# Performance work log

Measured on AMD Instinct MI355X. Metric: run time of the kernel, lower is better.

The kernel has to match this reference:

```python
import jax, jax.numpy as jnp
import numpy as np

B, T, S, C, H, F = 8, 1024, 256, 1024, 16, 4096
D = C // H  # head_dim = 64
EPS = 1e-5


def layernorm(x, g, b):
    mu = jnp.mean(x, axis=-1, keepdims=True)
    var = jnp.var(x, axis=-1, keepdims=True)
    return (x - mu) * jax.lax.rsqrt(var + EPS) * g + b


def setup_inputs() -> dict:
    key = jax.random.key(0)
    ks = jax.random.split(key, 16)
    s = lambda fan_in: 1.0 / np.sqrt(fan_in)
    return {
        "x": jax.random.normal(ks[0], (B, T, C), jnp.float32),
        "context": jax.random.normal(ks[1], (B, S, C), jnp.float32),
        # LayerNorms
        "ln1_g": jnp.ones((C,)), "ln1_b": jnp.zeros((C,)),
        "ln2_g": jnp.ones((C,)), "ln2_b": jnp.zeros((C,)),
        "ln3_g": jnp.ones((C,)), "ln3_b": jnp.zeros((C,)),
        # causal self-attention (qkv has no bias, proj has bias)
        "W_qkv": jax.random.normal(ks[2], (C, 3 * C), jnp.float32) * s(C),
        "W_sproj": jax.random.normal(ks[3], (C, C), jnp.float32) * s(C),
        "b_sproj": jnp.zeros((C,)),
        # cross-attention
        "W_q": jax.random.normal(ks[4], (C, C), jnp.float32) * s(C),
        "W_kv": jax.random.normal(ks[5], (C, 2 * C), jnp.float32) * s(C),
        "W_cproj": jax.random.normal(ks[6], (C, C), jnp.float32) * s(C),
        "b_cproj": jnp.zeros((C,)),
        # FFN
        "W_ff1": jax.random.normal(ks[7], (C, F), jnp.float32) * s(C),
        "b_ff1": jnp.zeros((F,)),
        "W_ff2": jax.random.normal(ks[8], (F, C), jnp.float32) * s(F),
        "b_ff2": jnp.zeros((C,)),
    }


def _split_heads(t):  # [B, L, C] -> [B, H, L, D]
    return t.reshape(t.shape[0], t.shape[1], H, D).transpose(0, 2, 1, 3)


def _merge_heads(t):  # [B, H, L, D] -> [B, L, C]
    return t.transpose(0, 2, 1, 3).reshape(t.shape[0], t.shape[2], C)


def gpt_block(x, context, ln1_g, ln1_b, ln2_g, ln2_b, ln3_g, ln3_b,
              W_qkv, W_sproj, b_sproj, W_q, W_kv, W_cproj, b_cproj,
              W_ff1, b_ff1, W_ff2, b_ff2):
    scale = 1.0 / np.sqrt(D)

    # --- causal self-attention (pre-norm) ---
    h = layernorm(x, ln1_g, ln1_b)
    qkv = h @ W_qkv                       # [B, T, 3C]
    q, k, v = jnp.split(qkv, 3, axis=-1)
    q, k, v = _split_heads(q), _split_heads(k), _split_heads(v)
    attn = jnp.einsum("bhtd,bhsd->bhts", q, k) * scale   # [B, H, T, T]
    causal = jnp.tril(jnp.ones((T, T), dtype=bool))
    attn = jnp.where(causal, attn, -jnp.inf)
    attn = jax.nn.softmax(attn, axis=-1)
    out = jnp.einsum("bhts,bhsd->bhtd", attn, v)
    x = x + (_merge_heads(out) @ W_sproj + b_sproj)

    # --- cross-attention (pre-norm) ---
    h = layernorm(x, ln2_g, ln2_b)
    q = _split_heads(h @ W_q)             # [B, H, T, D]
    kv = context @ W_kv                   # [B, S, 2C]
    k, v = jnp.split(kv, 2, axis=-1)
    k, v = _split_heads(k), _split_heads(v)
    attn = jax.nn.softmax(jnp.einsum("bhtd,bhsd->bhts", q, k) * scale, axis=-1)
    out = jnp.einsum("bhts,bhsd->bhtd", attn, v)
    x = x + (_merge_heads(out) @ W_cproj + b_cproj)

    # --- FFN (pre-norm, exact GELU) ---
    h = layernorm(x, ln3_g, ln3_b)
    h = jax.nn.gelu(h @ W_ff1 + b_ff1, approximate=False)
    x = x + (h @ W_ff2 + b_ff2)
    return x


def reference(x, context, ln1_g, ln1_b, ln2_g, ln2_b, ln3_g, ln3_b,
              W_qkv, W_sproj, b_sproj, W_q, W_kv, W_cproj, b_cproj,
              W_ff1, b_ff1, W_ff2, b_ff2):
    return gpt_block(x, context, ln1_g, ln1_b, ln2_g, ln2_b, ln3_g, ln3_b,
                     W_qkv, W_sproj, b_sproj, W_q, W_kv, W_cproj, b_cproj,
                     W_ff1, b_ff1, W_ff2, b_ff2)
```

## Files before the change

### kernel.cpp

```cpp
#include <hip/hip_runtime.h>
#include <math.h>

constexpr int B_ = 8, T_ = 1024, S_ = 256, C_ = 1024, H_ = 16, F_ = 4096, D_ = 64;

typedef __attribute__((ext_vector_type(8))) short bf16x8;
typedef __attribute__((ext_vector_type(8))) unsigned short ushort8;
typedef __attribute__((ext_vector_type(4))) unsigned short ushort4v;
typedef __attribute__((ext_vector_type(4))) float f32x4;

__device__ __forceinline__ unsigned short f2bf(float f) {
  union { float f; unsigned u; } c; c.f = f;
  unsigned u = c.u;
  u += 0x7FFFu + ((u >> 16) & 1u);
  return (unsigned short)(u >> 16);
}

__device__ __forceinline__ void gload16(const void* g, void* l) {
  typedef __attribute__((address_space(3))) unsigned int lds_u32;
  typedef __attribute__((address_space(1))) const unsigned int glb_u32;
  __builtin_amdgcn_global_load_lds((glb_u32*)(size_t)g,
                                   (lds_u32*)(unsigned)(size_t)l, 16, 0, 0);
}

__device__ __forceinline__ float gelu_fast(float v) {
  return v / (1.0f + __expf(-1.5957691216057308f * v * (1.0f + 0.044715f * v * v)));
}

__global__ __launch_bounds__(256) void ln_kernel(
    const float* __restrict__ x, const float* __restrict__ g,
    const float* __restrict__ b, unsigned short* __restrict__ out) {
  const int row = blockIdx.x;
  const int t = threadIdx.x;
  const float4 v = reinterpret_cast<const float4*>(x + (size_t)row * C_)[t];
  float sum = v.x + v.y + v.z + v.w;
  float ss  = v.x * v.x + v.y * v.y + v.z * v.z + v.w * v.w;
#pragma unroll
  for (int o = 1; o < 64; o <<= 1) {
    sum += __shfl_xor(sum, o);
    ss  += __shfl_xor(ss, o);
  }
  __shared__ float s1[4], s2[4];
  const int wid = t >> 6;
  if ((t & 63) == 0) { s1[wid] = sum; s2[wid] = ss; }
  __syncthreads();
  sum = s1[0] + s1[1] + s1[2] + s1[3];
  ss  = s2[0] + s2[1] + s2[2] + s2[3];
  const float inv = 1.0f / (float)C_;
  const float mu  = sum * inv;
  const float var = ss * inv - mu * mu;
  const float rstd = rsqrtf(var + 1e-5f);
  const float4 gg = reinterpret_cast<const float4*>(g)[t];
  const float4 bb = reinterpret_cast<const float4*>(b)[t];
  ushort4v o4;
  o4[0] = f2bf((v.x - mu) * rstd * gg.x + bb.x);
  o4[1] = f2bf((v.y - mu) * rstd * gg.y + bb.y);
  o4[2] = f2bf((v.z - mu) * rstd * gg.z + bb.z);
  o4[3] = f2bf((v.w - mu) * rstd * gg.w + bb.w);
  *reinterpret_cast<ushort4v*>(out + (size_t)row * C_ + t * 4) = o4;
}

__global__ __launch_bounds__(256) void wconvT_kernel(
    const float* __restrict__ W, unsigned short* __restrict__ Wt, int K, int N) {
  __shared__ unsigned short Lt[64][72];
  const int tid = threadIdx.x;
  const int n0 = blockIdx.x * 64, k0 = blockIdx.y * 64;
#pragma unroll
  for (int j = 0; j < 4; ++j) {
    const int kk = j * 16 + (tid >> 4);
    const float4 v = *reinterpret_cast<const float4*>(W + (size_t)(k0 + kk) * N + n0 + (tid & 15) * 4);
    const int nn = (tid & 15) * 4;
    Lt[nn + 0][kk] = f2bf(v.x);
    Lt[nn + 1][kk] = f2bf(v.y);
    Lt[nn + 2][kk] = f2bf(v.z);
    Lt[nn + 3][kk] = f2bf(v.w);
  }
  __syncthreads();
  const int rr = tid >> 3, ck = tid & 7;
#pragma unroll
  for (int j = 0; j < 2; ++j) {
    const int n = j * 32 + rr;
    *reinterpret_cast<ushort8*>(Wt + (size_t)(n0 + n) * K + k0 + ck * 8) =
        *reinterpret_cast<const ushort8*>(&Lt[n][ck * 8]);
  }
}

__global__ __launch_bounds__(256) void f2bf_kernel(
    const float* __restrict__ in, unsigned short* __restrict__ o, int n8) {
  const int i = blockIdx.x * 256 + threadIdx.x;
  if (i < n8) {
    const float4 a = *reinterpret_cast<const float4*>(in + (size_t)i * 8);
    const float4 b = *reinterpret_cast<const float4*>(in + (size_t)i * 8 + 4);
    ushort8 r;
    r[0] = f2bf(a.x); r[1] = f2bf(a.y); r[2] = f2bf(a.z); r[3] = f2bf(a.w);
    r[4] = f2bf(b.x); r[5] = f2bf(b.y); r[6] = f2bf(b.z); r[7] = f2bf(b.w);
    *reinterpret_cast<ushort8*>(o + (size_t)i * 8) = r;
  }
}

__global__ __launch_bounds__(256) void vtrans_kernel(
    const unsigned short* __restrict__ src, unsigned short* __restrict__ dst,
    int ldsrc, int Ts) {
  __shared__ unsigned short Lt[64][72];
  const int tid = threadIdx.x;
  const int bh = blockIdx.y, b = bh >> 4, h = bh & 15;
  const int t0 = blockIdx.x * 64;
  const int rr = tid >> 3, ck = tid & 7;
#pragma unroll
  for (int j = 0; j < 2; ++j) {
    const int t = j * 32 + rr;
    const ushort8 v = *reinterpret_cast<const ushort8*>(
        src + (size_t)(b * Ts + t0 + t) * ldsrc + h * 64 + ck * 8);
#pragma unroll
    for (int e = 0; e < 8; ++e) Lt[ck * 8 + e][t] = v[e];
  }
  __syncthreads();
#pragma unroll
  for (int j = 0; j < 2; ++j) {
    const int d = j * 32 + rr;
    *reinterpret_cast<ushort8*>(dst + ((size_t)bh * 64 + d) * Ts + t0 + ck * 8) =
        *reinterpret_cast<const ushort8*>(&Lt[d][ck * 8]);
  }
}

enum { EPI_NONE = 0, EPI_BIAS_RESID = 1, EPI_BIAS_GELU = 2 };

template <int EPI>
__global__ __launch_bounds__(256) void gemm_bf16(
    const unsigned short* __restrict__ A, const unsigned short* __restrict__ Bt,
    const float* __restrict__ bias, const float* __restrict__ resid,
    void* __restrict__ Cout, int M, int N, int K) {
  __shared__ unsigned short As[2][128 * 32];
  __shared__ unsigned short Bs[2][128 * 32];
  const int tid = threadIdx.x;
  const int w = tid >> 6, lane = tid & 63;
  const int ql = lane & 15, g = lane >> 4;
  const int bm = blockIdx.y * 128, bn = blockIdx.x * 128;
  const int wr = w >> 1, wc = w & 1;

  f32x4 acc[4][4] = {};

  const int srow16 = lane >> 2;
  const int skb = lane & 3;

  auto STAGE = [&](int bu, int k0) {
#pragma unroll
    for (int i = 0; i < 2; ++i) {
      const int row = i * 64 + w * 16 + srow16;
      const int kb = skb ^ ((row >> 1) & 3);
      gload16(A + (size_t)(bm + row) * K + k0 + kb * 8,
              (void*)(As[bu] + (i * 64 + w * 16) * 32));
      gload16(Bt + (size_t)(bn + row) * K + k0 + kb * 8,
              (void*)(Bs[bu] + (i * 64 + w * 16) * 32));
    }
  };
  auto COMPUTE = [&](int bu) {
    bf16x8 af[4], bfr[4];
#pragma unroll
    for (int f = 0; f < 4; ++f) {
      const int ra = wr * 64 + f * 16 + ql;
      af[f] = *reinterpret_cast<const bf16x8*>(As[bu] + ra * 32 + (g ^ ((ra >> 1) & 3)) * 8);
      const int rb = wc * 64 + f * 16 + ql;
      bfr[f] = *reinterpret_cast<const bf16x8*>(Bs[bu] + rb * 32 + (g ^ ((rb >> 1) & 3)) * 8);
    }
#pragma unroll
    for (int mf = 0; mf < 4; ++mf)
#pragma unroll
      for (int nf = 0; nf < 4; ++nf)
        acc[mf][nf] = __builtin_amdgcn_mfma_f32_16x16x32_bf16(af[mf], bfr[nf], acc[mf][nf], 0, 0, 0);
  };

  STAGE(0, 0);
  __syncthreads();
  int cur = 0;
  const int NT = K >> 5;
  for (int t = 0; t < NT - 1; ++t) {
    STAGE(cur ^ 1, (t + 1) * 32);
    COMPUTE(cur);
    __syncthreads();
    cur ^= 1;
  }
  COMPUTE(cur);

  float b4[4];
  if (EPI != EPI_NONE) {
#pragma unroll
    for (int nf = 0; nf < 4; ++nf) b4[nf] = bias[bn + wc * 64 + nf * 16 + ql];
  }
#pragma unroll
  for (int mf = 0; mf < 4; ++mf) {
#pragma unroll
    for (int r = 0; r < 4; ++r) {
      const size_t m = (size_t)(bm + wr * 64 + mf * 16 + g * 4 + r);
      const int ncol = bn + wc * 64 + ql;
      if (EPI == EPI_BIAS_RESID) {
        float* op = (float*)Cout + m * N + ncol;
        const float* rp = resid + m * N + ncol;
#pragma unroll
        for (int nf = 0; nf < 4; ++nf)
          op[nf * 16] = acc[mf][nf][r] + b4[nf] + rp[nf * 16];
      } else {
        unsigned short* op = (unsigned short*)Cout + m * N + ncol;
#pragma unroll
        for (int nf = 0; nf < 4; ++nf) {
          float v = acc[mf][nf][r];
          if (EPI == EPI_BIAS_GELU) v = gelu_fast(v + b4[nf]);
          op[nf * 16] = f2bf(v);
        }
      }
    }
  }
}

template <bool CAUSAL>
__global__ __launch_bounds__(256) void attn_mfma(
    const unsigned short* __restrict__ Qb, const unsigned short* __restrict__ Kb,
    const unsigned short* __restrict__ Vt, unsigned short* __restrict__ Ob,
    int Tk, int ldq, int ldk) {
  __shared__ unsigned short Ks[2][64 * 64];
  __shared__ unsigned short Vs[2][64 * 64];
  __shared__ unsigned short Pt[64][72];
  const int tid = threadIdx.x;
  const int w = tid >> 6, lane = tid & 63;
  const int ql = lane & 15, g = lane >> 4;
  const int bh = blockIdx.y, b = bh >> 4, h = bh & 15;
  const int qt = blockIdx.x;
  const int qrow = w * 16 + ql;
  const int qg = qt * 64 + qrow;

  bf16x8 qf0, qf1;
  {
    const unsigned short* qr = Qb + (size_t)(b * T_ + qg) * ldq + h * 64;
    qf0 = *reinterpret_cast<const bf16x8*>(qr + g * 8);
    qf1 = *reinterpret_cast<const bf16x8*>(qr + 32 + g * 8);
  }
  float m_run = -INFINITY, l_run = 0.f;
  f32x4 oacc[4] = {};

  const int nt = CAUSAL ? (qt + 1) : (Tk >> 6);
  const int srow = lane >> 3, skb = lane & 7;

  auto STAGE_KV = [&](int bu, int kt) {
#pragma unroll
    for (int i = 0; i < 2; ++i) {
      const int rloc = i * 32 + w * 8 + srow;
      const int kb = skb ^ (rloc & 7);
      gload16(Kb + (size_t)(b * Tk + kt * 64 + rloc) * ldk + h * 64 + kb * 8,
              (void*)(Ks[bu] + (i * 32 + w * 8) * 64));
      gload16(Vt + ((size_t)bh * 64 + rloc) * Tk + kt * 64 + kb * 8,
              (void*)(Vs[bu] + (i * 32 + w * 8) * 64));
    }
  };

  STAGE_KV(0, 0);
  __syncthreads();
  int cur = 0;

  for (int kt = 0; kt < nt; ++kt) {
    if (kt + 1 < nt) STAGE_KV(cur ^ 1, kt + 1);

    f32x4 sacc[4] = {};
#pragma unroll
    for (int kf = 0; kf < 4; ++kf) {
      const int kr = kf * 16 + ql;
      const int sw = ql & 7;
      const bf16x8 k0v = *reinterpret_cast<const bf16x8*>(Ks[cur] + kr * 64 + ((0 + g) ^ sw) * 8);
      const bf16x8 k1v = *reinterpret_cast<const bf16x8*>(Ks[cur] + kr * 64 + ((4 + g) ^ sw) * 8);
      sacc[kf] = __builtin_amdgcn_mfma_f32_16x16x32_bf16(k0v, qf0, sacc[kf], 0, 0, 0);
      sacc[kf] = __builtin_amdgcn_mfma_f32_16x16x32_bf16(k1v, qf1, sacc[kf], 0, 0, 0);
    }

    float sc[4][4];
    float tmax = -INFINITY;
#pragma unroll
    for (int kf = 0; kf < 4; ++kf)
#pragma unroll
      for (int r = 0; r < 4; ++r) {
        float v = sacc[kf][r] * 0.125f;
        if (CAUSAL) {
          const int key = kt * 64 + kf * 16 + g * 4 + r;
          if (key > qg) v = -INFINITY;
        }
        sc[kf][r] = v;
        tmax = fmaxf(tmax, v);
      }
    tmax = fmaxf(tmax, __shfl_xor(tmax, 16));
    tmax = fmaxf(tmax, __shfl_xor(tmax, 32));
    const float mnew = fmaxf(m_run, tmax);
    const float scl = __expf(m_run - mnew);
    float psum = 0.f;
    unsigned short pb[4][4];
#pragma unroll
    for (int kf = 0; kf < 4; ++kf)
#pragma unroll
      for (int r = 0; r < 4; ++r) {
        const float p = __expf(sc[kf][r] - mnew);
        psum += p;
        pb[kf][r] = f2bf(p);
      }
    psum += __shfl_xor(psum, 16);
    psum += __shfl_xor(psum, 32);
    l_run = l_run * scl + psum;
    m_run = mnew;
#pragma unroll
    for (int df = 0; df < 4; ++df)
#pragma unroll
      for (int r = 0; r < 4; ++r) oacc[df][r] *= scl;
#pragma unroll
    for (int kf = 0; kf < 4; ++kf) {
      ushort4v p4; p4[0] = pb[kf][0]; p4[1] = pb[kf][1]; p4[2] = pb[kf][2]; p4[3] = pb[kf][3];
      *reinterpret_cast<ushort4v*>(&Pt[qrow][kf * 16 + g * 4]) = p4;
    }
    asm volatile("s_waitcnt lgkmcnt(0)" ::: "memory");
    __builtin_amdgcn_s_barrier();

    const bf16x8 p0 = *reinterpret_cast<const bf16x8*>(&Pt[qrow][g * 8]);
    const bf16x8 p1 = *reinterpret_cast<const bf16x8*>(&Pt[qrow][32 + g * 8]);
#pragma unroll
    for (int df = 0; df < 4; ++df) {
      const int vr = df * 16 + ql;
      const int sw = ql & 7;
      const bf16x8 v0 = *reinterpret_cast<const bf16x8*>(Vs[cur] + vr * 64 + ((0 + g) ^ sw) * 8);
      const bf16x8 v1 = *reinterpret_cast<const bf16x8*>(Vs[cur] + vr * 64 + ((4 + g) ^ sw) * 8);
      oacc[df] = __builtin_amdgcn_mfma_f32_16x16x32_bf16(v0, p0, oacc[df], 0, 0, 0);
      oacc[df] = __builtin_amdgcn_mfma_f32_16x16x32_bf16(v1, p1, oacc[df], 0, 0, 0);
    }
    __syncthreads();
    cur ^= 1;
  }

  const float linv = 1.0f / l_run;
  unsigned short* orow = Ob + (size_t)(b * T_ + qg) * C_ + h * 64;
#pragma unroll
  for (int df = 0; df < 4; ++df)
#pragma unroll
    for (int r = 0; r < 4; ++r)
      orow[df * 16 + g * 4 + r] = f2bf(oacc[df][r] * linv);
}

extern "C" void kernel_launch(void* const* d_in, const int* in_sizes, int n_in,
                              void* d_out, int out_size, void* d_ws, size_t ws_size,
                              hipStream_t stream) {
  const float* x    = (const float*)d_in[0];
  const float* ctx  = (const float*)d_in[1];
  const float* ln1g = (const float*)d_in[2];
  const float* ln1b = (const float*)d_in[3];
  const float* ln2g = (const float*)d_in[4];
  const float* ln2b = (const float*)d_in[5];
  const float* ln3g = (const float*)d_in[6];
  const float* ln3b = (const float*)d_in[7];
  const float* Wqkv = (const float*)d_in[8];
  const float* Wsp  = (const float*)d_in[9];
  const float* bsp  = (const float*)d_in[10];
  const float* Wq   = (const float*)d_in[11];
  const float* Wkv  = (const float*)d_in[12];
  const float* Wcp  = (const float*)d_in[13];
  const float* bcp  = (const float*)d_in[14];
  const float* Wf1  = (const float*)d_in[15];
  const float* bf1  = (const float*)d_in[16];
  const float* Wf2  = (const float*)d_in[17];
  const float* bf2  = (const float*)d_in[18];
  float* out = (float*)d_out;

  char* wsb = (char*)d_ws;
  unsigned short* WqkvT = (unsigned short*)(wsb + 0);
  unsigned short* WspT  = (unsigned short*)(wsb + 6291456);
  unsigned short* WqT   = (unsigned short*)(wsb + 8388608);
  unsigned short* WkvT  = (unsigned short*)(wsb + 10485760);
  unsigned short* WcpT  = (unsigned short*)(wsb + 14680064);
  unsigned short* Wf1T  = (unsigned short*)(wsb + 16777216);
  unsigned short* Wf2T  = (unsigned short*)(wsb + 25165824);
  unsigned short* ctxb  = (unsigned short*)(wsb + 33554432);
  unsigned short* lnout = (unsigned short*)(wsb + 37748736);
  unsigned short* attno = (unsigned short*)(wsb + 54525952);
  char* regA = wsb + 71303168;
  unsigned short* qkvb = (unsigned short*)regA;
  unsigned short* VtS  = (unsigned short*)(regA + 50331648);
  unsigned short* qbuf = (unsigned short*)regA;
  unsigned short* kvb  = (unsigned short*)(regA + 16777216);
  unsigned short* VtC  = (unsigned short*)(regA + 25165824);
  unsigned short* ff1o = (unsigned short*)regA;

  const dim3 blk(256);

  wconvT_kernel<<<dim3(48, 16), blk, 0, stream>>>(Wqkv, WqkvT, 1024, 3072);
  wconvT_kernel<<<dim3(16, 16), blk, 0, stream>>>(Wsp, WspT, 1024, 1024);
  wconvT_kernel<<<dim3(16, 16), blk, 0, stream>>>(Wq, WqT, 1024, 1024);
  wconvT_kernel<<<dim3(32, 16), blk, 0, stream>>>(Wkv, WkvT, 1024, 2048);
  wconvT_kernel<<<dim3(16, 16), blk, 0, stream>>>(Wcp, WcpT, 1024, 1024);
  wconvT_kernel<<<dim3(64, 16), blk, 0, stream>>>(Wf1, Wf1T, 1024, 4096);
  wconvT_kernel<<<dim3(16, 64), blk, 0, stream>>>(Wf2, Wf2T, 4096, 1024);
  f2bf_kernel<<<1024, blk, 0, stream>>>(ctx, ctxb, 262144);

  ln_kernel<<<8192, blk, 0, stream>>>(x, ln1g, ln1b, lnout);
  gemm_bf16<EPI_NONE><<<dim3(24, 64), blk, 0, stream>>>(
      lnout, WqkvT, nullptr, nullptr, qkvb, 8192, 3072, 1024);
  vtrans_kernel<<<dim3(16, 128), blk, 0, stream>>>(qkvb + 2048, VtS, 3072, 1024);
  attn_mfma<true><<<dim3(16, 128), blk, 0, stream>>>(
      qkvb, qkvb + 1024, VtS, attno, 1024, 3072, 3072);
  gemm_bf16<EPI_BIAS_RESID><<<dim3(8, 64), blk, 0, stream>>>(
      attno, WspT, bsp, x, out, 8192, 1024, 1024);

  ln_kernel<<<8192, blk, 0, stream>>>(out, ln2g, ln2b, lnout);
  gemm_bf16<EPI_NONE><<<dim3(8, 64), blk, 0, stream>>>(
      lnout, WqT, nullptr, nullptr, qbuf, 8192, 1024, 1024);
  gemm_bf16<EPI_NONE><<<dim3(16, 16), blk, 0, stream>>>(
      ctxb, WkvT, nullptr, nullptr, kvb, 2048, 2048, 1024);
  vtrans_kernel<<<dim3(4, 128), blk, 0, stream>>>(kvb + 1024, VtC, 2048, 256);
  attn_mfma<false><<<dim3(16, 128), blk, 0, stream>>>(
      qbuf, kvb, VtC, attno, 256, 1024, 2048);
  gemm_bf16<EPI_BIAS_RESID><<<dim3(8, 64), blk, 0, stream>>>(
      attno, WcpT, bcp, out, out, 8192, 1024, 1024);

  ln_kernel<<<8192, blk, 0, stream>>>(out, ln3g, ln3b, lnout);
  gemm_bf16<EPI_BIAS_GELU><<<dim3(32, 64), blk, 0, stream>>>(
      lnout, Wf1T, bf1, nullptr, ff1o, 8192, 4096, 1024);
  gemm_bf16<EPI_BIAS_RESID><<<dim3(8, 64), blk, 0, stream>>>(
      ff1o, Wf2T, bf2, out, out, 8192, 1024, 4096);
}
```

Baseline: 693.5 us.

## Replace GEMM with 256-row tiled, 512-thread, BK=64 kernel with XCD swizzle

Every projection GEMM now uses a new kernel with 256xBN block tiles, 8 waves, a K-step of 64 and an XOR-swizzled LDS layout. The kernel also waits on explicit vmcnt counts for the double-buffered direct-to-LDS loads, raises wave priority around MFMA bursts, and remaps block IDs so neighbouring tiles land on the same XCD. The aim is more data reuse per block, fewer barriers per unit of K, and better L2 locality. The cost is higher LDS use (up to 128KB), more register pressure, and fewer blocks for the small GEMMs.

```diff
diff --git a/kernel.cpp b/kernel.cpp
--- a/kernel.cpp
+++ b/kernel.cpp
@@ -124,74 +124,121 @@
 
 enum { EPI_NONE = 0, EPI_BIAS_RESID = 1, EPI_BIAS_GELU = 2 };
 
-template <int EPI>
-__global__ __launch_bounds__(256) void gemm_bf16(
+template <int EPI, int BN_, int WM, int WN>
+__global__ __launch_bounds__(512) void gemm256(
     const unsigned short* __restrict__ A, const unsigned short* __restrict__ Bt,
     const float* __restrict__ bias, const float* __restrict__ resid,
     void* __restrict__ Cout, int M, int N, int K) {
-  __shared__ unsigned short As[2][128 * 32];
-  __shared__ unsigned short Bs[2][128 * 32];
+  static_assert(WM * WN == 8, "");
+  constexpr int MR = 256 / WM;
+  constexpr int NR = BN_ / WN;
+  constexpr int MFR = MR / 16;
+  static_assert(NR == 64, "");
+  constexpr int B_ISS = BN_ / 64;
+  constexpr int NS = 4 + B_ISS;
+
+  __shared__ unsigned short As[2][256 * 64];
+  __shared__ unsigned short Bs[2][BN_ * 64];
+
   const int tid = threadIdx.x;
   const int w = tid >> 6, lane = tid & 63;
   const int ql = lane & 15, g = lane >> 4;
-  const int bm = blockIdx.y * 128, bn = blockIdx.x * 128;
-  const int wr = w >> 1, wc = w & 1;
-
-  f32x4 acc[4][4] = {};
-
-  const int srow16 = lane >> 2;
-  const int skb = lane & 3;
+  const int wr = w / WN, wc = w % WN;
+
+  const int nbx = gridDim.x;
+  const int nwg = gridDim.x * gridDim.y;
+  const int orig = blockIdx.y * nbx + blockIdx.x;
+  const int swz = (orig & 7) * (nwg >> 3) + (orig >> 3);
+  const int bm = (swz / nbx) * 256;
+  const int bn = (swz % nbx) * BN_;
+
+  f32x4 acc[MFR][4] = {};
 
   auto STAGE = [&](int bu, int k0) {
-#pragma unroll
-    for (int i = 0; i < 2; ++i) {
-      const int row = i * 64 + w * 16 + srow16;
-      const int kb = skb ^ ((row >> 1) & 3);
-      gload16(A + (size_t)(bm + row) * K + k0 + kb * 8,
-              (void*)(As[bu] + (i * 64 + w * 16) * 32));
-      gload16(Bt + (size_t)(bn + row) * K + k0 + kb * 8,
-              (void*)(Bs[bu] + (i * 64 + w * 16) * 32));
+    char* aDst = (char*)&As[bu][0] + w * 1024;
+    char* bDst = (char*)&Bs[bu][0] + w * 1024;
+#pragma unroll
+    for (int i = 0; i < 4; ++i) {
+      const unsigned L = i * 8192u + (unsigned)tid * 16u;
+      const int row = (int)(L >> 7);
+      const unsigned kb = (L & 127u) ^ ((unsigned)(row & 7) << 4);
+      gload16(A + (size_t)(bm + row) * K + k0 + (kb >> 1), aDst + i * 8192);
+    }
+#pragma unroll
+    for (int i = 0; i < B_ISS; ++i) {
+      const unsigned L = i * 8192u + (unsigned)tid * 16u;
+      const int row = (int)(L >> 7);
+      const unsigned kb = (L & 127u) ^ ((unsigned)(row & 7) << 4);
+      gload16(Bt + (size_t)(bn + row) * K + k0 + (kb >> 1), bDst + i * 8192);
     }
   };
-  auto COMPUTE = [&](int bu) {
-    bf16x8 af[4], bfr[4];
-#pragma unroll
-    for (int f = 0; f < 4; ++f) {
-      const int ra = wr * 64 + f * 16 + ql;
-      af[f] = *reinterpret_cast<const bf16x8*>(As[bu] + ra * 32 + (g ^ ((ra >> 1) & 3)) * 8);
-      const int rb = wc * 64 + f * 16 + ql;
-      bfr[f] = *reinterpret_cast<const bf16x8*>(Bs[bu] + rb * 32 + (g ^ ((rb >> 1) & 3)) * 8);
-    }
-#pragma unroll
-    for (int mf = 0; mf < 4; ++mf)
-#pragma unroll
-      for (int nf = 0; nf < 4; ++nf)
-        acc[mf][nf] = __builtin_amdgcn_mfma_f32_16x16x32_bf16(af[mf], bfr[nf], acc[mf][nf], 0, 0, 0);
-  };
 
   STAGE(0, 0);
-  __syncthreads();
   int cur = 0;
-  const int NT = K >> 5;
-  for (int t = 0; t < NT - 1; ++t) {
-    STAGE(cur ^ 1, (t + 1) * 32);
-    COMPUTE(cur);
-    __syncthreads();
+  const int NT = K >> 6;
+  for (int t = 0; t < NT; ++t) {
+    if (t + 1 < NT) {
+      STAGE(cur ^ 1, (t + 1) * 64);
+      if constexpr (NS == 8) asm volatile("s_waitcnt vmcnt(8)" ::: "memory");
+      else                   asm volatile("s_waitcnt vmcnt(6)" ::: "memory");
+    } else {
+      asm volatile("s_waitcnt vmcnt(0)" ::: "memory");
+    }
+    __builtin_amdgcn_s_barrier();
+
+    const char* aBase = (const char*)&As[cur][0];
+    const char* bBase = (const char*)&Bs[cur][0];
+#pragma unroll
+    for (int mh = 0; mh < MFR / 4; ++mh) {
+      bf16x8 a0[4], a1[4];
+#pragma unroll
+      for (int m4 = 0; m4 < 4; ++m4) {
+        const int row = wr * MR + (mh * 4 + m4) * 16 + ql;
+        const unsigned sw = (unsigned)(row & 7) << 4;
+        a0[m4] = *(const bf16x8*)(aBase + row * 128 + (unsigned)((g * 16) ^ sw));
+        a1[m4] = *(const bf16x8*)(aBase + row * 128 + (unsigned)((64 + g * 16) ^ sw));
+      }
+#pragma unroll
+      for (int nh = 0; nh < 2; ++nh) {
+        bf16x8 b0[2], b1[2];
+#pragma unroll
+        for (int n2 = 0; n2 < 2; ++n2) {
+          const int rowb = wc * NR + (nh * 2 + n2) * 16 + ql;
+          const unsigned sw = (unsigned)(rowb & 7) << 4;
+          b0[n2] = *(const bf16x8*)(bBase + rowb * 128 + (unsigned)((g * 16) ^ sw));
+          b1[n2] = *(const bf16x8*)(bBase + rowb * 128 + (unsigned)((64 + g * 16) ^ sw));
+        }
+        __builtin_amdgcn_s_barrier();
+        asm volatile("s_waitcnt lgkmcnt(0)" ::: "memory");
+        __builtin_amdgcn_sched_barrier(0);
+        __builtin_amdgcn_s_setprio(1);
+#pragma unroll
+        for (int m4 = 0; m4 < 4; ++m4)
+#pragma unroll
+          for (int n2 = 0; n2 < 2; ++n2) {
+            acc[mh * 4 + m4][nh * 2 + n2] = __builtin_amdgcn_mfma_f32_16x16x32_bf16(
+                a0[m4], b0[n2], acc[mh * 4 + m4][nh * 2 + n2], 0, 0, 0);
+            acc[mh * 4 + m4][nh * 2 + n2] = __builtin_amdgcn_mfma_f32_16x16x32_bf16(
+                a1[m4], b1[n2], acc[mh * 4 + m4][nh * 2 + n2], 0, 0, 0);
+          }
+        __builtin_amdgcn_s_setprio(0);
+        __builtin_amdgcn_s_barrier();
+      }
+    }
     cur ^= 1;
   }
-  COMPUTE(cur);
 
   float b4[4];
   if (EPI != EPI_NONE) {
 #pragma unroll
-    for (int nf = 0; nf < 4; ++nf) b4[nf] = bias[bn + wc * 64 + nf * 16 + ql];
-  }
-#pragma unroll
-  for (int mf = 0; mf < 4; ++mf) {
+    for (int nf = 0; nf < 4; ++nf) b4[nf] = bias[bn + wc * NR + nf * 16 + ql];
+  }
+#pragma unroll
+  for (int mf = 0; mf < MFR; ++mf) {
 #pragma unroll
     for (int r = 0; r < 4; ++r) {
-      const size_t m = (size_t)(bm + wr * 64 + mf * 16 + g * 4 + r);
-      const int ncol = bn + wc * 64 + ql;
+      const size_t m = (size_t)(bm + wr * MR + mf * 16 + g * 4 + r);
+      const int ncol = bn + wc * NR + ql;
       if (EPI == EPI_BIAS_RESID) {
         float* op = (float*)Cout + m * N + ncol;
         const float* rp = resid + m * N + ncol;
@@ -381,6 +428,7 @@
   unsigned short* ff1o = (unsigned short*)regA;
 
   const dim3 blk(256);
+  const dim3 blk512(512);
 
   wconvT_kernel<<<dim3(48, 16), blk, 0, stream>>>(Wqkv, WqkvT, 1024, 3072);
   wconvT_kernel<<<dim3(16, 16), blk, 0, stream>>>(Wsp, WspT, 1024, 1024);
@@ -392,28 +440,28 @@
   f2bf_kernel<<<1024, blk, 0, stream>>>(ctx, ctxb, 262144);
 
   ln_kernel<<<8192, blk, 0, stream>>>(x, ln1g, ln1b, lnout);
-  gemm_bf16<EPI_NONE><<<dim3(24, 64), blk, 0, stream>>>(
+  gemm256<EPI_NONE, 256, 2, 4><<<dim3(12, 32), blk512, 0, stream>>>(
       lnout, WqkvT, nullptr, nullptr, qkvb, 8192, 3072, 1024);
   vtrans_kernel<<<dim3(16, 128), blk, 0, stream>>>(qkvb + 2048, VtS, 3072, 1024);
   attn_mfma<true><<<dim3(16, 128), blk, 0, stream>>>(
       qkvb, qkvb + 1024, VtS, attno, 1024, 3072, 3072);
-  gemm_bf16<EPI_BIAS_RESID><<<dim3(8, 64), blk, 0, stream>>>(
+  gemm256<EPI_BIAS_RESID, 128, 4, 2><<<dim3(8, 32), blk512, 0, stream>>>(
       attno, WspT, bsp, x, out, 8192, 1024, 1024);
 
   ln_kernel<<<8192, blk, 0, stream>>>(out, ln2g, ln2b, lnout);
-  gemm_bf16<EPI_NONE><<<dim3(8, 64), blk, 0, stream>>>(
+  gemm256<EPI_NONE, 128, 4, 2><<<dim3(8, 32), blk512, 0, stream>>>(
       lnout, WqT, nullptr, nullptr, qbuf, 8192, 1024, 1024);
-  gemm_bf16<EPI_NONE><<<dim3(16, 16), blk, 0, stream>>>(
+  gemm256<EPI_NONE, 128, 4, 2><<<dim3(16, 8), blk512, 0, stream>>>(
       ctxb, WkvT, nullptr, nullptr, kvb, 2048, 2048, 1024);
   vtrans_kernel<<<dim3(4, 128), blk, 0, stream>>>(kvb + 1024, VtC, 2048, 256);
   attn_mfma<false><<<dim3(16, 128), blk, 0, stream>>>(
       qbuf, kvb, VtC, attno, 256, 1024, 2048);
-  gemm_bf16<EPI_BIAS_RESID><<<dim3(8, 64), blk, 0, stream>>>(
+  gemm256<EPI_BIAS_RESID, 128, 4, 2><<<dim3(8, 32), blk512, 0, stream>>>(
       attno, WcpT, bcp, out, out, 8192, 1024, 1024);
 
   ln_kernel<<<8192, blk, 0, stream>>>(out, ln3g, ln3b, lnout);
-  gemm_bf16<EPI_BIAS_GELU><<<dim3(32, 64), blk, 0, stream>>>(
+  gemm256<EPI_BIAS_GELU, 256, 2, 4><<<dim3(16, 32), blk512, 0, stream>>>(
       lnout, Wf1T, bf1, nullptr, ff1o, 8192, 4096, 1024);
-  gemm_bf16<EPI_BIAS_RESID><<<dim3(8, 64), blk, 0, stream>>>(
+  gemm256<EPI_BIAS_RESID, 128, 4, 2><<<dim3(8, 32), blk512, 0, stream>>>(
       ff1o, Wf2T, bf2, out, out, 8192, 1024, 4096);
 }
```

Measured after the change: 659.3 us. -4.9%, faster.
